# Optimization experiments

Hardware: AMD Instinct MI355X
Metric: run time of the kernel (lower is better)

The kernel has to match this reference:

```python
import jax, jax.numpy as jnp
import numpy as np

N, E, G = 4096, 16384, 16
IN_C, EDGE_C, H = 3, 4, 128
LN_EPS = 1e-5


def setup_inputs() -> dict:
    key = jax.random.key(0)
    ks = jax.random.split(key, 32)
    nrm = lambda k, shp, s: jax.random.normal(k, shp, jnp.float32) * s
    inp = {}
    inp["x"] = nrm(ks[0], (N, IN_C), 1.0)
    inp["edge_index"] = jax.random.randint(ks[1], (2, E), 0, N)
    inp["edge_attr"] = nrm(ks[2], (E, EDGE_C), 1.0)
    inp["batch"] = jnp.sort(jax.random.randint(ks[3], (N,), 0, G))
    inp["contingency_type"] = nrm(ks[4], (G, 4), 1.0)
    inp["load_scale"] = nrm(ks[5], (G,), 1.0)
    i = 6
    def conv_params(prefix, in_c):
        nonlocal i
        inp[prefix + "_w1"] = nrm(ks[i], (EDGE_C, 128), 1.0 / np.sqrt(EDGE_C)); i += 1
        inp[prefix + "_b1"] = jnp.zeros((128,), jnp.float32)
        inp[prefix + "_w2"] = nrm(ks[i], (128, in_c * H), 1.0 / np.sqrt(128)); i += 1
        inp[prefix + "_b2"] = jnp.zeros((in_c * H,), jnp.float32)
        inp[prefix + "_root"] = nrm(ks[i], (in_c, H), 1.0 / np.sqrt(in_c)); i += 1
        inp[prefix + "_bias"] = jnp.zeros((H,), jnp.float32)
    conv_params("c1", IN_C)
    conv_params("c2", H)
    conv_params("c3", H)
    for p in ("ln1", "ln2", "ln3"):
        inp[p + "_g"] = jnp.ones((H,), jnp.float32)
        inp[p + "_b"] = jnp.zeros((H,), jnp.float32)
    inp["lin_w"] = nrm(ks[i], (2 * H + 4 + 1, 2), 1.0 / np.sqrt(2 * H + 5)); i += 1
    inp["lin_b"] = jnp.zeros((2,), jnp.float32)
    return inp


def _nnconv(x, src, dst, edge_attr, w1, b1, w2, b2, root, bias, in_c):
    # edge MLP -> per-edge weight matrix [E, in_c, H]
    h = jax.nn.relu(edge_attr @ w1 + b1)
    W = (h @ w2 + b2).reshape(-1, in_c, H)
    msg = jnp.einsum('ei,eio->eo', x[src], W)  # gather + per-edge matmul
    s = jax.ops.segment_sum(msg, dst, num_segments=N)
    cnt = jax.ops.segment_sum(jnp.ones((msg.shape[0],), msg.dtype), dst, num_segments=N)
    agg = s / jnp.maximum(cnt, 1.0)[:, None]  # scatter-mean
    return agg + x @ root + bias


def _layernorm(x, g, b):
    m = jnp.mean(x, axis=-1, keepdims=True)
    v = jnp.mean(jnp.square(x - m), axis=-1, keepdims=True)
    return (x - m) * jax.lax.rsqrt(v + LN_EPS) * g + b


def reference(x, edge_index, edge_attr, batch, contingency_type, load_scale,
              c1_w1, c1_b1, c1_w2, c1_b2, c1_root, c1_bias,
              c2_w1, c2_b1, c2_w2, c2_b2, c2_root, c2_bias,
              c3_w1, c3_b1, c3_w2, c3_b2, c3_root, c3_bias,
              ln1_g, ln1_b, ln2_g, ln2_b, ln3_g, ln3_b,
              lin_w, lin_b):
    src, dst = edge_index[0], edge_index[1]
    h = _nnconv(x, src, dst, edge_attr, c1_w1, c1_b1, c1_w2, c1_b2, c1_root, c1_bias, IN_C)
    h = jax.nn.relu(_layernorm(h, ln1_g, ln1_b))
    h = _nnconv(h, src, dst, edge_attr, c2_w1, c2_b1, c2_w2, c2_b2, c2_root, c2_bias, H)
    h = jax.nn.elu(_layernorm(h, ln2_g, ln2_b))
    h = _nnconv(h, src, dst, edge_attr, c3_w1, c3_b1, c3_w2, c3_b2, c3_root, c3_bias, H)
    h = jax.nn.leaky_relu(_layernorm(h, ln3_g, ln3_b), negative_slope=0.01)
    # global mean / max pool over graphs
    gsum = jax.ops.segment_sum(h, batch, num_segments=G)
    gcnt = jax.ops.segment_sum(jnp.ones((N,), h.dtype), batch, num_segments=G)
    gmean = gsum / jnp.maximum(gcnt, 1.0)[:, None]
    gmax = jax.ops.segment_max(h, batch, num_segments=G)
    gmax = jnp.where(gcnt[:, None] > 0, gmax, 0.0)
    x_cat = jnp.concatenate([gmean, gmax, contingency_type, load_scale[:, None]], axis=1)
    return x_cat @ lin_w + lin_b
```

## Files before the change

kernel.cpp:

```cpp
#include <hip/hip_runtime.h>
#include <hip/hip_bf16.h>


#define N_NODES 4096
#define N_EDGES 16384
#define N_GRAPHS 16
#define HD 128
#define BM 128
#define LDB 136
#define KSPLIT 2
#define KT_PER (HD / KSPLIT)
#define SLAB_E (HD * HD)
#define PN 32

typedef unsigned short ushort_t;
typedef __attribute__((ext_vector_type(8))) short short8;
typedef __attribute__((ext_vector_type(4))) float f32x4;

static __device__ __forceinline__ ushort_t f2b(float f) {
    __hip_bfloat16 h = __float2bfloat16(f);
    union { __hip_bfloat16 h; ushort_t u; } cv; cv.h = h; return cv.u;
}
static __device__ __forceinline__ float b2f(ushort_t u) {
    union { unsigned u; float f; } cv; cv.u = ((unsigned)u) << 16; return cv.f;
}

static __device__ __forceinline__ float wave_sum(float v) {
#pragma unroll
    for (int off = 1; off < 64; off <<= 1) v += __shfl_xor(v, off, 64);
    return v;
}

__global__ __launch_bounds__(256) void count_feat(
    const int* __restrict__ src, const int* __restrict__ dst, const float* __restrict__ x,
    float* __restrict__ cnt, float* __restrict__ sfeat) {
    int e = blockIdx.x * 256 + threadIdx.x;
    int d = dst[e], s = src[e];
    atomicAdd(&cnt[d], 1.0f);
    atomicAdd(&sfeat[d * 4 + 0], x[s * 3 + 0]);
    atomicAdd(&sfeat[d * 4 + 1], x[s * 3 + 1]);
    atomicAdd(&sfeat[d * 4 + 2], x[s * 3 + 2]);
}

__global__ __launch_bounds__(256) void w2r_prep(const float* __restrict__ w2,
                                                ushort_t* __restrict__ w2r) {
    __shared__ ushort_t tile[HD][LDB];
    const int i = blockIdx.x;
    const int t = threadIdx.x;
    for (int c = 0; c < 64; ++c) {
        int flat = c * 256 + t;
        int k = flat >> 7, o = flat & 127;
        tile[o][k] = f2b(w2[k * 384 + i * HD + o]);
    }
    __syncthreads();
    uint4* outp = (uint4*)(w2r + (size_t)i * SLAB_E);
    for (int it = 0; it < 8; ++it) {
        int c = it * 256 + t;
        int ng = c >> 9, j = (c >> 6) & 7, l = c & 63;
        int ni = j >> 2, kb = j & 3;
        int R  = ng * 32 + ni * 16 + (l & 15);
        int ke = kb * 32 + (l >> 4) * 8;
        outp[c] = *(const uint4*)&tile[R][ke];
    }
}

__global__ __launch_bounds__(512, 2) void l1_gemm(
    const float* __restrict__ x, const int* __restrict__ src, const int* __restrict__ dst,
    const float* __restrict__ ea, const float* __restrict__ w1, const float* __restrict__ b1,
    const ushort_t* __restrict__ w2r, float* __restrict__ agg) {
    __shared__ ushort_t Hs[SLAB_E];
    __shared__ float    XV[3][BM];

    const int t = threadIdx.x;
    const int lane = t & 63, quad = lane >> 4, l16 = lane & 15;
    const int wave = t >> 6;
    const int mg = wave >> 2;
    const int ng = wave & 3;
    const int e0 = blockIdx.x * BM;
    const int rbase = mg * 64;

    {
        const int e = t & 127;
        const int kb32 = (t >> 7) * 32;
        const float4 av = ((const float4*)ea)[e0 + e];
        if (t < 128) {
            const int n = src[e0 + t];
            XV[0][t] = x[n * 3 + 0]; XV[1][t] = x[n * 3 + 1]; XV[2][t] = x[n * 3 + 2];
        }
        const int r7 = e & 7;
        ushort_t* hrow = Hs + e * HD;
#pragma unroll
        for (int c = 0; c < 4; ++c) {
            const int kbase = kb32 + c * 8;
            unsigned pk0, pk1, pk2, pk3;
#pragma unroll
            for (int u = 0; u < 4; ++u) {
                const int ka = kbase + 2 * u, kb = ka + 1;
                float s0 = b1[ka];
                s0 = fmaf(av.x, w1[0 * HD + ka], s0);
                s0 = fmaf(av.y, w1[1 * HD + ka], s0);
                s0 = fmaf(av.z, w1[2 * HD + ka], s0);
                s0 = fmaf(av.w, w1[3 * HD + ka], s0);
                float s1 = b1[kb];
                s1 = fmaf(av.x, w1[0 * HD + kb], s1);
                s1 = fmaf(av.y, w1[1 * HD + kb], s1);
                s1 = fmaf(av.z, w1[2 * HD + kb], s1);
                s1 = fmaf(av.w, w1[3 * HD + kb], s1);
                unsigned pr = (unsigned)f2b(fmaxf(s0, 0.0f)) |
                              ((unsigned)f2b(fmaxf(s1, 0.0f)) << 16);
                if (u == 0) pk0 = pr; else if (u == 1) pk1 = pr;
                else if (u == 2) pk2 = pr; else pk3 = pr;
            }
            uint4 v; v.x = pk0; v.y = pk1; v.z = pk2; v.w = pk3;
            *(uint4*)&hrow[(((kbase >> 3) ^ r7) << 3)] = v;
        }
    }
    __syncthreads();

    short8 afrag[4][4];
#pragma unroll
    for (int mi = 0; mi < 4; ++mi) {
        const int R = rbase + mi * 16 + l16;
        const ushort_t* rowp = Hs + R * HD;
        const int r7 = R & 7;
#pragma unroll
        for (int kb = 0; kb < 4; ++kb)
            afrag[mi][kb] = *(const short8*)&rowp[((kb * 4 + quad) ^ r7) << 3];
    }

    f32x4 acc[4][2];
#pragma unroll
    for (int mi = 0; mi < 4; ++mi)
#pragma unroll
        for (int ni = 0; ni < 2; ++ni)
            acc[mi][ni] = (f32x4){0.f, 0.f, 0.f, 0.f};

    const ushort_t* bbase = w2r + (size_t)ng * 4096 + (size_t)lane * 8;

#define LOADB(bf, slab)                                                         \
    {                                                                           \
        const ushort_t* bw = bbase + (size_t)(slab) * SLAB_E;                   \
        _Pragma("unroll") for (int ni = 0; ni < 2; ++ni)                        \
            _Pragma("unroll") for (int kb = 0; kb < 4; ++kb)                    \
                bf[ni][kb] = *(const short8*)(bw + (ni * 4 + kb) * 512);        \
    }
#define CONSUME_XV(bf, i)                                                       \
    {                                                                           \
        _Pragma("unroll") for (int mi = 0; mi < 4; ++mi) {                      \
            float4 xv = *(const float4*)&XV[i][rbase + mi * 16 + quad * 4];     \
            _Pragma("unroll") for (int ni = 0; ni < 2; ++ni) {                  \
                f32x4 p = {0.f, 0.f, 0.f, 0.f};                                 \
                _Pragma("unroll") for (int kb = 0; kb < 4; ++kb)                \
                    p = __builtin_amdgcn_mfma_f32_16x16x32_bf16(                \
                        afrag[mi][kb], bf[ni][kb], p, 0, 0, 0);                 \
                acc[mi][ni][0] = fmaf(xv.x, p[0], acc[mi][ni][0]);              \
                acc[mi][ni][1] = fmaf(xv.y, p[1], acc[mi][ni][1]);              \
                acc[mi][ni][2] = fmaf(xv.z, p[2], acc[mi][ni][2]);              \
                acc[mi][ni][3] = fmaf(xv.w, p[3], acc[mi][ni][3]);              \
            }                                                                   \
        }                                                                       \
    }

    short8 bfA[2][4], bfB[2][4];
    LOADB(bfA, 0);
    LOADB(bfB, 1);
    CONSUME_XV(bfA, 0);
    LOADB(bfA, 2);
    CONSUME_XV(bfB, 1);
    CONSUME_XV(bfA, 2);
#undef LOADB
#undef CONSUME_XV

#pragma unroll
    for (int mi = 0; mi < 4; ++mi) {
#pragma unroll
        for (int r = 0; r < 4; ++r) {
            const int dn = dst[e0 + rbase + mi * 16 + quad * 4 + r];
#pragma unroll
            for (int ni = 0; ni < 2; ++ni)
                atomicAdd(&agg[dn * HD + ng * 32 + ni * 16 + l16], acc[mi][ni][r]);
        }
    }
}

__global__ __launch_bounds__(128) void node_update_l1(
    float* __restrict__ agg, const float* __restrict__ cnt, const float* __restrict__ sfeat,
    const float* __restrict__ x, const float* __restrict__ root, const float* __restrict__ bias,
    const float* __restrict__ b2, const float* __restrict__ lng, const float* __restrict__ lnb) {
    const int n = blockIdx.x, o = threadIdx.x;
    float s = bias[o];
#pragma unroll
    for (int i = 0; i < 3; ++i) s = fmaf(x[n * 3 + i], root[i * HD + o], s);
    float sb = 0.0f;
#pragma unroll
    for (int i = 0; i < 3; ++i) sb = fmaf(sfeat[n * 4 + i], b2[i * HD + o], sb);
    float v = (agg[n * HD + o] + sb) / fmaxf(cnt[n], 1.0f) + s;
    __shared__ float red[2];
    float ws = wave_sum(v);
    if ((o & 63) == 0) red[o >> 6] = ws;
    __syncthreads();
    float m = (red[0] + red[1]) * (1.0f / HD);
    float d = v - m;
    float ws2 = wave_sum(d * d);
    __syncthreads();
    if ((o & 63) == 0) red[o >> 6] = ws2;
    __syncthreads();
    float var = (red[0] + red[1]) * (1.0f / HD);
    float y = d * rsqrtf(var + 1e-5f) * lng[o] + lnb[o];
    agg[n * HD + o] = fmaxf(y, 0.0f);
}

__global__ __launch_bounds__(256) void w2t_prep(const float* __restrict__ w2,
                                                const float* __restrict__ b2,
                                                ushort_t* __restrict__ w2t) {
    __shared__ ushort_t tile[HD][LDB];
    const int kt = blockIdx.x;
    const int t = threadIdx.x;
    const float* srcp = (kt < HD) ? (w2 + kt * HD * HD) : b2;
    for (int c = 0; c < 64; ++c) {
        int flat = c * 256 + t;
        int i = flat >> 7, o = flat & 127;
        tile[o][i] = f2b(srcp[i * HD + o]);
    }
    __syncthreads();
    uint4* outp = (uint4*)(w2t + (size_t)kt * SLAB_E);
    for (int it = 0; it < 8; ++it) {
        int c = it * 256 + t;
        int ng = c >> 9, j = (c >> 6) & 7, l = c & 63;
        int ni = j >> 2, kb = j & 3;
        int R  = ng * 32 + ni * 16 + (l & 15);
        int ke = kb * 32 + (l >> 4) * 8;
        outp[c] = *(const uint4*)&tile[R][ke];
    }
}

__global__ __launch_bounds__(512, 2) void gemm_mfma(
    const float* __restrict__ hprev, const float* __restrict__ ea,
    const float* __restrict__ w1, const float* __restrict__ b1,
    const ushort_t* __restrict__ w2t,
    const int* __restrict__ src, const int* __restrict__ dst,
    float* __restrict__ agg) {
    __shared__ ushort_t Xs[SLAB_E];
    __shared__ ushort_t HeT[KT_PER][BM];

    const int t = threadIdx.x;
    const int lane = t & 63, quad = lane >> 4, l16 = lane & 15;
    const int wave = t >> 6;
    const int mg = wave >> 2;
    const int ng = wave & 3;
    const int eb = blockIdx.x >> 1;
    const int ks = blockIdx.x & 1;
    const int k0 = ks * KT_PER;
    const int e0 = eb * BM;
    const int rbase = mg * 64;

    {
        const int le = t >> 2;
        const int j0 = (t & 3) * 4;
        const int r7 = le & 7;
        const float* rp = hprev + src[e0 + le] * HD + (t & 3) * 32;
        ushort_t* xrow = Xs + le * HD;
#pragma unroll
        for (int c = 0; c < 4; ++c) {
            float4 va = ((const float4*)rp)[2 * c];
            float4 vb = ((const float4*)rp)[2 * c + 1];
            uint4 pk;
            pk.x = (unsigned)f2b(va.x) | ((unsigned)f2b(va.y) << 16);
            pk.y = (unsigned)f2b(va.z) | ((unsigned)f2b(va.w) << 16);
            pk.z = (unsigned)f2b(vb.x) | ((unsigned)f2b(vb.y) << 16);
            pk.w = (unsigned)f2b(vb.z) | ((unsigned)f2b(vb.w) << 16);
            *(uint4*)&xrow[((j0 + c) ^ r7) << 3] = pk;
        }
    }

    {
        const int e = t & 127;
        const float4 av = ((const float4*)ea)[e0 + e];
        for (int kl = t >> 7; kl < KT_PER; kl += 4) {
            const int kt = k0 + kl;
            float s = b1[kt];
            s = fmaf(av.x, w1[0 * HD + kt], s);
            s = fmaf(av.y, w1[1 * HD + kt], s);
            s = fmaf(av.z, w1[2 * HD + kt], s);
            s = fmaf(av.w, w1[3 * HD + kt], s);
            HeT[kl][e] = f2b(fmaxf(s, 0.0f));
        }
    }
    __syncthreads();

    short8 afrag[4][4];
#pragma unroll
    for (int mi = 0; mi < 4; ++mi) {
        const int R = rbase + mi * 16 + l16;
        const ushort_t* rowp = Xs + R * HD;
        const int r7 = R & 7;
#pragma unroll
        for (int kb = 0; kb < 4; ++kb)
            afrag[mi][kb] = *(const short8*)&rowp[((kb * 4 + quad) ^ r7) << 3];
    }

    f32x4 acc[4][2];
#pragma unroll
    for (int mi = 0; mi < 4; ++mi)
#pragma unroll
        for (int ni = 0; ni < 2; ++ni)
            acc[mi][ni] = (f32x4){0.f, 0.f, 0.f, 0.f};

    const ushort_t* bbase = w2t + (size_t)ng * 4096 + (size_t)lane * 8;

#define LOADB(bf, slab)                                                         \
    {                                                                           \
        const ushort_t* bw = bbase + (size_t)(slab) * SLAB_E;                   \
        _Pragma("unroll") for (int ni = 0; ni < 2; ++ni)                        \
            _Pragma("unroll") for (int kb = 0; kb < 4; ++kb)                    \
                bf[ni][kb] = *(const short8*)(bw + (ni * 4 + kb) * 512);        \
    }
#define CONSUME(bf, s)                                                          \
    {                                                                           \
        _Pragma("unroll") for (int mi = 0; mi < 4; ++mi) {                      \
            ushort4 hv = *(const ushort4*)&HeT[s][rbase + mi * 16 + quad * 4];  \
            float h0 = b2f(hv.x), h1 = b2f(hv.y), h2 = b2f(hv.z), h3 = b2f(hv.w);\
            _Pragma("unroll") for (int ni = 0; ni < 2; ++ni) {                  \
                f32x4 p = {0.f, 0.f, 0.f, 0.f};                                 \
                _Pragma("unroll") for (int kb = 0; kb < 4; ++kb)                \
                    p = __builtin_amdgcn_mfma_f32_16x16x32_bf16(                \
                        afrag[mi][kb], bf[ni][kb], p, 0, 0, 0);                 \
                acc[mi][ni][0] = fmaf(h0, p[0], acc[mi][ni][0]);                \
                acc[mi][ni][1] = fmaf(h1, p[1], acc[mi][ni][1]);                \
                acc[mi][ni][2] = fmaf(h2, p[2], acc[mi][ni][2]);                \
                acc[mi][ni][3] = fmaf(h3, p[3], acc[mi][ni][3]);                \
            }                                                                   \
        }                                                                       \
    }

    short8 bfA[2][4], bfB[2][4];
    LOADB(bfA, k0);
    for (int s = 0; s < KT_PER; s += 2) {
        LOADB(bfB, k0 + s + 1);
        CONSUME(bfA, s);
        __builtin_amdgcn_s_barrier();
        if (s + 2 < KT_PER) LOADB(bfA, k0 + s + 2)
        else if (ks == 1)   LOADB(bfA, HD);
        CONSUME(bfB, s + 1);
        __builtin_amdgcn_s_barrier();
    }
    if (ks == 1) {
#pragma unroll
        for (int mi = 0; mi < 4; ++mi)
#pragma unroll
            for (int ni = 0; ni < 2; ++ni) {
                f32x4 p = {0.f, 0.f, 0.f, 0.f};
#pragma unroll
                for (int kb = 0; kb < 4; ++kb)
                    p = __builtin_amdgcn_mfma_f32_16x16x32_bf16(
                        afrag[mi][kb], bfA[ni][kb], p, 0, 0, 0);
                acc[mi][ni][0] += p[0]; acc[mi][ni][1] += p[1];
                acc[mi][ni][2] += p[2]; acc[mi][ni][3] += p[3];
            }
    }
#undef LOADB
#undef CONSUME

#pragma unroll
    for (int mi = 0; mi < 4; ++mi) {
#pragma unroll
        for (int r = 0; r < 4; ++r) {
            const int dn = dst[e0 + rbase + mi * 16 + quad * 4 + r];
#pragma unroll
            for (int ni = 0; ni < 2; ++ni)
                atomicAdd(&agg[dn * HD + ng * 32 + ni * 16 + l16], acc[mi][ni][r]);
        }
    }
}

__global__ __launch_bounds__(128) void node_update(
    float* __restrict__ agg, const float* __restrict__ cnt,
    const float* __restrict__ hprev, const float* __restrict__ root, const float* __restrict__ bias,
    const float* __restrict__ lng, const float* __restrict__ lnb, int act) {
    const int n = blockIdx.x, o = threadIdx.x;
    __shared__ float hr[HD];
    hr[o] = hprev[n * HD + o];
    __syncthreads();
    float s = bias[o];
#pragma unroll 8
    for (int k = 0; k < HD; ++k) s = fmaf(hr[k], root[k * HD + o], s);
    float v = agg[n * HD + o] / fmaxf(cnt[n], 1.0f) + s;
    __shared__ float red[2];
    float ws = wave_sum(v);
    if ((o & 63) == 0) red[o >> 6] = ws;
    __syncthreads();
    float m = (red[0] + red[1]) * (1.0f / HD);
    float d = v - m;
    float ws2 = wave_sum(d * d);
    __syncthreads();
    if ((o & 63) == 0) red[o >> 6] = ws2;
    __syncthreads();
    float var = (red[0] + red[1]) * (1.0f / HD);
    float y = d * rsqrtf(var + 1e-5f) * lng[o] + lnb[o];
    if (act == 1) y = (y > 0.0f) ? y : expm1f(y);
    else y = (y > 0.0f) ? y : 0.01f * y;
    agg[n * HD + o] = y;
}

static __device__ __forceinline__ unsigned fkey(float f) {
    unsigned b = __float_as_uint(f);
    return (b & 0x80000000u) ? ~b : (b | 0x80000000u);
}
__global__ __launch_bounds__(128) void pool_scatter(
    const float* __restrict__ h3, const int* __restrict__ batch,
    float* __restrict__ gsum, unsigned* __restrict__ gmaxk, int* __restrict__ gcnt) {
    const int o = threadIdx.x;
    const int nb = blockIdx.x * PN;
    float sum = 0.0f, mx = -3.0e38f;
    int gcur = batch[nb];
    int run = 0;
    for (int j = 0; j < PN; ++j) {
        const int n = nb + j;
        const int g = batch[n];
        const float v = h3[n * HD + o];
        if (g != gcur) {
            atomicAdd(&gsum[gcur * HD + o], sum);
            atomicMax(&gmaxk[gcur * HD + o], fkey(mx));
            if (o == 0) atomicAdd(&gcnt[gcur], run);
            sum = 0.0f; mx = -3.0e38f; run = 0; gcur = g;
        }
        sum += v; mx = fmaxf(mx, v); ++run;
    }
    atomicAdd(&gsum[gcur * HD + o], sum);
    atomicMax(&gmaxk[gcur * HD + o], fkey(mx));
    if (o == 0) atomicAdd(&gcnt[gcur], run);
}

__global__ __launch_bounds__(128) void pool_head2(
    const float* __restrict__ gsum, const unsigned* __restrict__ gmaxk, const int* __restrict__ gcnt,
    const float* __restrict__ cont, const float* __restrict__ ls,
    const float* __restrict__ lin_w, const float* __restrict__ lin_b, float* __restrict__ out) {
    const int g = blockIdx.x, o = threadIdx.x;
    const int c = gcnt[g];
    __shared__ float xcat[2 * HD + 5];
    xcat[o] = gsum[g * HD + o] / fmaxf((float)c, 1.0f);
    unsigned key = gmaxk[g * HD + o];
    unsigned bits = (key & 0x80000000u) ? (key & 0x7FFFFFFFu) : ~key;
    xcat[HD + o] = (c > 0) ? __uint_as_float(bits) : 0.0f;
    if (o < 4) xcat[2 * HD + o] = cont[g * 4 + o];
    if (o == 0) xcat[2 * HD + 4] = ls[g];
    __syncthreads();
    if (o < 2) {
        float r = lin_b[o];
        for (int ri = 0; ri < 2 * HD + 5; ++ri) r = fmaf(xcat[ri], lin_w[ri * 2 + o], r);
        out[g * 2 + o] = r;
    }
}

extern "C" void kernel_launch(void* const* d_in, const int* in_sizes, int n_in,
                              void* d_out, int out_size, void* d_ws, size_t ws_size,
                              hipStream_t stream) {
    const float* x     = (const float*)d_in[0];
    const int*   ei    = (const int*)d_in[1];
    const float* ea    = (const float*)d_in[2];
    const int*   batch = (const int*)d_in[3];
    const float* cont  = (const float*)d_in[4];
    const float* ls    = (const float*)d_in[5];
    const float *c1_w1 = (const float*)d_in[6],  *c1_b1 = (const float*)d_in[7];
    const float *c1_w2 = (const float*)d_in[8],  *c1_b2 = (const float*)d_in[9];
    const float *c1_rt = (const float*)d_in[10], *c1_bs = (const float*)d_in[11];
    const float *c2_w1 = (const float*)d_in[12], *c2_b1 = (const float*)d_in[13];
    const float *c2_w2 = (const float*)d_in[14], *c2_b2 = (const float*)d_in[15];
    const float *c2_rt = (const float*)d_in[16], *c2_bs = (const float*)d_in[17];
    const float *c3_w1 = (const float*)d_in[18], *c3_b1 = (const float*)d_in[19];
    const float *c3_w2 = (const float*)d_in[20], *c3_b2 = (const float*)d_in[21];
    const float *c3_rt = (const float*)d_in[22], *c3_bs = (const float*)d_in[23];
    const float *ln1g = (const float*)d_in[24], *ln1b = (const float*)d_in[25];
    const float *ln2g = (const float*)d_in[26], *ln2b = (const float*)d_in[27];
    const float *ln3g = (const float*)d_in[28], *ln3b = (const float*)d_in[29];
    const float *lin_w = (const float*)d_in[30], *lin_b = (const float*)d_in[31];
    float* out = (float*)d_out;

    float*    cnt   = (float*)d_ws;
    float*    sfeat = cnt + N_NODES;
    float*    bufA  = sfeat + 4 * N_NODES;
    float*    bufB  = bufA + N_NODES * HD;
    ushort_t* w2t   = (ushort_t*)(bufB + N_NODES * HD);
    float*    gsum  = (float*)(w2t + (HD + 1) * HD * HD);
    unsigned* gmaxk = (unsigned*)(gsum + N_GRAPHS * HD);
    int*      gcnt  = (int*)(gmaxk + N_GRAPHS * HD);
    const int* src = ei;
    const int* dst = ei + N_EDGES;

    hipMemsetAsync(cnt, 0, 5 * N_NODES * sizeof(float), stream);
    count_feat<<<N_EDGES / 256, 256, 0, stream>>>(src, dst, x, cnt, sfeat);

    w2r_prep<<<3, 256, 0, stream>>>(c1_w2, w2t);
    hipMemsetAsync(bufA, 0, N_NODES * HD * sizeof(float), stream);
    l1_gemm<<<N_EDGES / BM, 512, 0, stream>>>(x, src, dst, ea, c1_w1, c1_b1, w2t, bufA);
    node_update_l1<<<N_NODES, 128, 0, stream>>>(bufA, cnt, sfeat, x, c1_rt, c1_bs, c1_b2, ln1g, ln1b);

    w2t_prep<<<HD + 1, 256, 0, stream>>>(c2_w2, c2_b2, w2t);
    hipMemsetAsync(bufB, 0, N_NODES * HD * sizeof(float), stream);
    gemm_mfma<<<(N_EDGES / BM) * KSPLIT, 512, 0, stream>>>(bufA, ea, c2_w1, c2_b1, w2t, src, dst, bufB);
    node_update<<<N_NODES, 128, 0, stream>>>(bufB, cnt, bufA, c2_rt, c2_bs, ln2g, ln2b, 1);

    w2t_prep<<<HD + 1, 256, 0, stream>>>(c3_w2, c3_b2, w2t);
    hipMemsetAsync(bufA, 0, N_NODES * HD * sizeof(float), stream);
    gemm_mfma<<<(N_EDGES / BM) * KSPLIT, 512, 0, stream>>>(bufB, ea, c3_w1, c3_b1, w2t, src, dst, bufA);
    node_update<<<N_NODES, 128, 0, stream>>>(bufA, cnt, bufB, c3_rt, c3_bs, ln3g, ln3b, 2);

    hipMemsetAsync(gsum, 0, (2 * N_GRAPHS * HD + N_GRAPHS) * sizeof(float), stream);
    pool_scatter<<<N_NODES / PN, 128, 0, stream>>>(bufA, batch, gsum, gmaxk, gcnt);
    pool_head2<<<N_GRAPHS, 128, 0, stream>>>(gsum, gmaxk, gcnt, cont, ls, lin_w, lin_b, out);
}
```

Before: 368.8 us.

## Fuse prep kernels, merge memsets, and fold pooling into final node update

Merges the edge-count/feature scatter and the layer-1 weight repacking into one launch. It replaces several separate memsets with a single workspace-wide memset. The layer-2 node update now zeroes the previous buffer so it can serve as layer-3's aggregation target. The final node update also performs graph mean/max pooling directly with per-node atomics, removing a separate pooling kernel. This cuts launch and memset overhead, but adds heavy atomic contention on the per-graph accumulators (many nodes per graph hitting the same addresses). It also zeroes a larger region than needed, including the bf16 weight buffer.

Measured after the change: 390.0 us. 5.8% more time.

```diff
diff --git a/kernel.cpp b/kernel.cpp
--- a/kernel.cpp
+++ b/kernel.cpp
@@ -11,7 +11,6 @@
 #define KSPLIT 2
 #define KT_PER (HD / KSPLIT)
 #define SLAB_E (HD * HD)
-#define PN 32
 
 typedef unsigned short ushort_t;
 typedef __attribute__((ext_vector_type(8))) short short8;
@@ -31,36 +30,37 @@
     return v;
 }
 
-__global__ __launch_bounds__(256) void count_feat(
+__global__ __launch_bounds__(256) void prep1(
     const int* __restrict__ src, const int* __restrict__ dst, const float* __restrict__ x,
-    float* __restrict__ cnt, float* __restrict__ sfeat) {
-    int e = blockIdx.x * 256 + threadIdx.x;
-    int d = dst[e], s = src[e];
-    atomicAdd(&cnt[d], 1.0f);
-    atomicAdd(&sfeat[d * 4 + 0], x[s * 3 + 0]);
-    atomicAdd(&sfeat[d * 4 + 1], x[s * 3 + 1]);
-    atomicAdd(&sfeat[d * 4 + 2], x[s * 3 + 2]);
-}
-
-__global__ __launch_bounds__(256) void w2r_prep(const float* __restrict__ w2,
-                                                ushort_t* __restrict__ w2r) {
+    float* __restrict__ cnt, float* __restrict__ sfeat,
+    const float* __restrict__ w2, ushort_t* __restrict__ w2r) {
     __shared__ ushort_t tile[HD][LDB];
-    const int i = blockIdx.x;
+    const int b = blockIdx.x;
     const int t = threadIdx.x;
-    for (int c = 0; c < 64; ++c) {
-        int flat = c * 256 + t;
-        int k = flat >> 7, o = flat & 127;
-        tile[o][k] = f2b(w2[k * 384 + i * HD + o]);
-    }
-    __syncthreads();
-    uint4* outp = (uint4*)(w2r + (size_t)i * SLAB_E);
-    for (int it = 0; it < 8; ++it) {
-        int c = it * 256 + t;
-        int ng = c >> 9, j = (c >> 6) & 7, l = c & 63;
-        int ni = j >> 2, kb = j & 3;
-        int R  = ng * 32 + ni * 16 + (l & 15);
-        int ke = kb * 32 + (l >> 4) * 8;
-        outp[c] = *(const uint4*)&tile[R][ke];
+    if (b < N_EDGES / 256) {
+        int e = b * 256 + t;
+        int d = dst[e], s = src[e];
+        atomicAdd(&cnt[d], 1.0f);
+        atomicAdd(&sfeat[d * 4 + 0], x[s * 3 + 0]);
+        atomicAdd(&sfeat[d * 4 + 1], x[s * 3 + 1]);
+        atomicAdd(&sfeat[d * 4 + 2], x[s * 3 + 2]);
+    } else {
+        const int i = b - N_EDGES / 256;
+        for (int c = 0; c < 64; ++c) {
+            int flat = c * 256 + t;
+            int k = flat >> 7, o = flat & 127;
+            tile[o][k] = f2b(w2[k * 384 + i * HD + o]);
+        }
+        __syncthreads();
+        uint4* outp = (uint4*)(w2r + (size_t)i * SLAB_E);
+        for (int it = 0; it < 8; ++it) {
+            int c = it * 256 + t;
+            int ng = c >> 9, j = (c >> 6) & 7, l = c & 63;
+            int ni = j >> 2, kb = j & 3;
+            int R  = ng * 32 + ni * 16 + (l & 15);
+            int ke = kb * 32 + (l >> 4) * 8;
+            outp[c] = *(const uint4*)&tile[R][ke];
+        }
     }
 }
 
@@ -375,8 +375,8 @@
 
 __global__ __launch_bounds__(128) void node_update(
     float* __restrict__ agg, const float* __restrict__ cnt,
-    const float* __restrict__ hprev, const float* __restrict__ root, const float* __restrict__ bias,
-    const float* __restrict__ lng, const float* __restrict__ lnb, int act) {
+    float* __restrict__ hprev, const float* __restrict__ root, const float* __restrict__ bias,
+    const float* __restrict__ lng, const float* __restrict__ lnb) {
     const int n = blockIdx.x, o = threadIdx.x;
     __shared__ float hr[HD];
     hr[o] = hprev[n * HD + o];
@@ -397,38 +397,46 @@
     __syncthreads();
     float var = (red[0] + red[1]) * (1.0f / HD);
     float y = d * rsqrtf(var + 1e-5f) * lng[o] + lnb[o];
-    if (act == 1) y = (y > 0.0f) ? y : expm1f(y);
-    else y = (y > 0.0f) ? y : 0.01f * y;
+    y = (y > 0.0f) ? y : expm1f(y);
     agg[n * HD + o] = y;
+    hprev[n * HD + o] = 0.0f;
 }
 
 static __device__ __forceinline__ unsigned fkey(float f) {
     unsigned b = __float_as_uint(f);
     return (b & 0x80000000u) ? ~b : (b | 0x80000000u);
 }
-__global__ __launch_bounds__(128) void pool_scatter(
-    const float* __restrict__ h3, const int* __restrict__ batch,
+__global__ __launch_bounds__(128) void node_update_pool(
+    const float* __restrict__ agg, const float* __restrict__ cnt,
+    const float* __restrict__ hprev, const float* __restrict__ root, const float* __restrict__ bias,
+    const float* __restrict__ lng, const float* __restrict__ lnb,
+    const int* __restrict__ batch,
     float* __restrict__ gsum, unsigned* __restrict__ gmaxk, int* __restrict__ gcnt) {
-    const int o = threadIdx.x;
-    const int nb = blockIdx.x * PN;
-    float sum = 0.0f, mx = -3.0e38f;
-    int gcur = batch[nb];
-    int run = 0;
-    for (int j = 0; j < PN; ++j) {
-        const int n = nb + j;
-        const int g = batch[n];
-        const float v = h3[n * HD + o];
-        if (g != gcur) {
-            atomicAdd(&gsum[gcur * HD + o], sum);
-            atomicMax(&gmaxk[gcur * HD + o], fkey(mx));
-            if (o == 0) atomicAdd(&gcnt[gcur], run);
-            sum = 0.0f; mx = -3.0e38f; run = 0; gcur = g;
-        }
-        sum += v; mx = fmaxf(mx, v); ++run;
-    }
-    atomicAdd(&gsum[gcur * HD + o], sum);
-    atomicMax(&gmaxk[gcur * HD + o], fkey(mx));
-    if (o == 0) atomicAdd(&gcnt[gcur], run);
+    const int n = blockIdx.x, o = threadIdx.x;
+    __shared__ float hr[HD];
+    hr[o] = hprev[n * HD + o];
+    __syncthreads();
+    float s = bias[o];
+#pragma unroll 8
+    for (int k = 0; k < HD; ++k) s = fmaf(hr[k], root[k * HD + o], s);
+    float v = agg[n * HD + o] / fmaxf(cnt[n], 1.0f) + s;
+    __shared__ float red[2];
+    float ws = wave_sum(v);
+    if ((o & 63) == 0) red[o >> 6] = ws;
+    __syncthreads();
+    float m = (red[0] + red[1]) * (1.0f / HD);
+    float d = v - m;
+    float ws2 = wave_sum(d * d);
+    __syncthreads();
+    if ((o & 63) == 0) red[o >> 6] = ws2;
+    __syncthreads();
+    float var = (red[0] + red[1]) * (1.0f / HD);
+    float y = d * rsqrtf(var + 1e-5f) * lng[o] + lnb[o];
+    y = (y > 0.0f) ? y : 0.01f * y;
+    const int g = batch[n];
+    atomicAdd(&gsum[g * HD + o], y);
+    atomicMax(&gmaxk[g * HD + o], fkey(y));
+    if (o == 0) atomicAdd(&gcnt[g], 1);
 }
 
 __global__ __launch_bounds__(128) void pool_head2(
@@ -487,25 +495,22 @@
     const int* src = ei;
     const int* dst = ei + N_EDGES;
 
-    hipMemsetAsync(cnt, 0, 5 * N_NODES * sizeof(float), stream);
-    count_feat<<<N_EDGES / 256, 256, 0, stream>>>(src, dst, x, cnt, sfeat);
-
-    w2r_prep<<<3, 256, 0, stream>>>(c1_w2, w2t);
-    hipMemsetAsync(bufA, 0, N_NODES * HD * sizeof(float), stream);
+    size_t ws_bytes = (size_t)((char*)(gcnt + N_GRAPHS) - (char*)d_ws);
+    hipMemsetAsync(d_ws, 0, ws_bytes, stream);
+
+    prep1<<<N_EDGES / 256 + 3, 256, 0, stream>>>(src, dst, x, cnt, sfeat, c1_w2, w2t);
+
     l1_gemm<<<N_EDGES / BM, 512, 0, stream>>>(x, src, dst, ea, c1_w1, c1_b1, w2t, bufA);
     node_update_l1<<<N_NODES, 128, 0, stream>>>(bufA, cnt, sfeat, x, c1_rt, c1_bs, c1_b2, ln1g, ln1b);
 
     w2t_prep<<<HD + 1, 256, 0, stream>>>(c2_w2, c2_b2, w2t);
-    hipMemsetAsync(bufB, 0, N_NODES * HD * sizeof(float), stream);
     gemm_mfma<<<(N_EDGES / BM) * KSPLIT, 512, 0, stream>>>(bufA, ea, c2_w1, c2_b1, w2t, src, dst, bufB);
-    node_update<<<N_NODES, 128, 0, stream>>>(bufB, cnt, bufA, c2_rt, c2_bs, ln2g, ln2b, 1);
+    node_update<<<N_NODES, 128, 0, stream>>>(bufB, cnt, bufA, c2_rt, c2_bs, ln2g, ln2b);
 
     w2t_prep<<<HD + 1, 256, 0, stream>>>(c3_w2, c3_b2, w2t);
-    hipMemsetAsync(bufA, 0, N_NODES * HD * sizeof(float), stream);
     gemm_mfma<<<(N_EDGES / BM) * KSPLIT, 512, 0, stream>>>(bufB, ea, c3_w1, c3_b1, w2t, src, dst, bufA);
-    node_update<<<N_NODES, 128, 0, stream>>>(bufA, cnt, bufB, c3_rt, c3_bs, ln3g, ln3b, 2);
-
-    hipMemsetAsync(gsum, 0, (2 * N_GRAPHS * HD + N_GRAPHS) * sizeof(float), stream);
-    pool_scatter<<<N_NODES / PN, 128, 0, stream>>>(bufA, batch, gsum, gmaxk, gcnt);
+    node_update_pool<<<N_NODES, 128, 0, stream>>>(bufA, cnt, bufB, c3_rt, c3_bs, ln3g, ln3b,
+                                                  batch, gsum, gmaxk, gcnt);
+
     pool_head2<<<N_GRAPHS, 128, 0, stream>>>(gsum, gmaxk, gcnt, cont, ls, lin_w, lin_b, out);
 }
```
